# Performance work log

Hardware: AMD Instinct MI355X
Metric: run time of the kernel (lower is better)

The kernel has to match this reference:

```python
import jax, jax.numpy as jnp
import numpy as np

N_NODES = 50000
N_EDGES = 800000
DIM = 128
LN_EPS = 1e-5


def setup_inputs() -> dict:
    key = jax.random.key(0)
    k1, k2, k3, k4 = jax.random.split(key, 4)
    h = jax.random.normal(k1, (N_NODES, DIM), dtype=jnp.float32)
    edge_index = jax.random.randint(k2, (2, N_EDGES), 0, N_NODES, dtype=jnp.int64)
    W = jax.random.normal(k3, (DIM, DIM), dtype=jnp.float32) / np.sqrt(DIM)
    b = jnp.zeros((DIM,), dtype=jnp.float32)
    gamma = jnp.ones((DIM,), dtype=jnp.float32)
    beta = jnp.zeros((DIM,), dtype=jnp.float32)
    t = jnp.zeros((), dtype=jnp.float32)
    return {"t": t, "h": h, "edge_index": edge_index, "batch_size": N_NODES,
            "W": W, "b": b, "gamma": gamma, "beta": beta}


def _gcn_conv(h, edge_index, W, b):
    """PyG-style GCNConv: D^{-1/2} (A+I) D^{-1/2} (h W) + b."""
    N = h.shape[0]
    loops = jnp.arange(N, dtype=edge_index.dtype)
    src = jnp.concatenate([edge_index[0], loops])  # [E+N]
    dst = jnp.concatenate([edge_index[1], loops])  # [E+N]
    # degree (with self loops) on destination nodes
    deg = jax.ops.segment_sum(jnp.ones_like(dst, dtype=h.dtype), dst, num_segments=N)
    dinv = jnp.where(deg > 0, jax.lax.rsqrt(deg), 0.0)
    norm = dinv[src] * dinv[dst]                    # [E+N]
    xw = h @ W                                      # [N, D]
    msg = xw[src] * norm[:, None]                   # gather + scale, [E+N, D]
    agg = jax.ops.segment_sum(msg, dst, num_segments=N)  # scatter-add, [N, D]
    return agg + b


def reference(t, h, edge_index, batch_size, W, b, gamma, beta):
    if h.ndim == 1:
        h = h[None, :]
    dh = _gcn_conv(h, edge_index, W, b)
    # LayerNorm over feature dim, then tanh
    mean = jnp.mean(dh, axis=-1, keepdims=True)
    var = jnp.mean(jnp.square(dh - mean), axis=-1, keepdims=True)
    dh = (dh - mean) * jax.lax.rsqrt(var + LN_EPS) * gamma + beta
    dh = jnp.tanh(dh)
    return (dh, jnp.zeros_like(edge_index), jnp.zeros_like(jnp.asarray(batch_size)))
```

## Files before the change

kernel.cpp:

```cpp
#include <hip/hip_runtime.h>
#include <math.h>

#define NN 50000
#define NE 800000
#define D  128
#define SCAN_CHUNK 1024
#define NSCAN ((NN + SCAN_CHUNK - 1) / SCAN_CHUNK)
#define PG_BLOCKS 782

typedef __attribute__((ext_vector_type(8))) short bf16x8;
typedef __attribute__((ext_vector_type(4))) float f32x4;

__device__ __forceinline__ unsigned short f32_to_bf16(float f) {
    unsigned u = __float_as_uint(f);
    u = u + 0x7FFFu + ((u >> 16) & 1u);
    return (unsigned short)(u >> 16);
}

__device__ __forceinline__ float fast_tanh(float x) {
    float e = __expf(2.0f * x);
    return fmaf(-2.0f, __builtin_amdgcn_rcpf(e + 1.0f), 1.0f);
}

__global__ __launch_bounds__(256) void k_init(
        const float* __restrict__ Wg, int* __restrict__ deg,
        unsigned short* __restrict__ wpk, unsigned short* __restrict__ zb) {
    int tid = threadIdx.x;
    int idx = blockIdx.x * 256 + tid;

    if (idx < 12500) ((int4*)deg)[idx] = (int4){0, 0, 0, 0};
    if (idx == 12500) deg[50000] = 0;

    if (blockIdx.x == 0) {
#pragma unroll 8
        for (int i = 0; i < 64; i++) {
            int o = i * 256 + tid;
            int j = o & 7, frag = o >> 3;
            int lo = frag & 15, quad = (frag >> 4) & 3;
            int kt = (frag >> 6) & 3, nt = frag >> 8;
            int k = kt * 32 + quad * 8 + j, n = nt * 16 + lo;
            wpk[o] = f32_to_bf16(Wg[k * 128 + n]);
        }
    }
    if (blockIdx.x == 1 && tid < 64)
        ((unsigned*)(zb + (size_t)NN * D))[tid] = 0u;
}

__global__ __launch_bounds__(256) void k_count_gemm(
        const float* __restrict__ h, const uint4* __restrict__ wpk4,
        const int* __restrict__ ei, int* __restrict__ deg,
        unsigned short* __restrict__ rank, float* __restrict__ zf,
        int* __restrict__ outtail, int tailN) {
    int tid = threadIdx.x;
    int bid = blockIdx.x;

    if (bid & 1) {
        int g = (bid >> 1) * 256 + tid;
        if (g < NE / 4) {
            int4 d4 = ((const int4*)(ei + NE))[g];
            ushort4 r;
            r.x = (unsigned short)atomicAdd(&deg[d4.x], 1);
            r.y = (unsigned short)atomicAdd(&deg[d4.y], 1);
            r.z = (unsigned short)atomicAdd(&deg[d4.z], 1);
            r.w = (unsigned short)atomicAdd(&deg[d4.w], 1);
            ((ushort4*)rank)[g] = r;
        }
        for (int i = g; i < tailN; i += PG_BLOCKS * 256) outtail[i] = 0;
        return;
    }

    int gid = bid >> 1;
    int w = tid >> 6, lane = tid & 63;
    int quad = lane >> 4, lo = lane & 15;
    int rowBase = gid * 64 + w * 16;
    int rowA = rowBase + lo; if (rowA > NN - 1) rowA = NN - 1;
    const float4* h4 = (const float4*)h;

    bf16x8 af[4];
#pragma unroll
    for (int kt = 0; kt < 4; kt++) {
        float4 u = h4[(size_t)rowA * 32 + kt * 8 + quad * 2];
        float4 v = h4[(size_t)rowA * 32 + kt * 8 + quad * 2 + 1];
        bf16x8 a;
        a[0] = (short)f32_to_bf16(u.x); a[1] = (short)f32_to_bf16(u.y);
        a[2] = (short)f32_to_bf16(u.z); a[3] = (short)f32_to_bf16(u.w);
        a[4] = (short)f32_to_bf16(v.x); a[5] = (short)f32_to_bf16(v.y);
        a[6] = (short)f32_to_bf16(v.z); a[7] = (short)f32_to_bf16(v.w);
        af[kt] = a;
    }

    f32x4 acc[8];
#pragma unroll
    for (int nt = 0; nt < 8; nt++) acc[nt] = (f32x4){0.f, 0.f, 0.f, 0.f};

#pragma unroll
    for (int kt = 0; kt < 4; kt++) {
#pragma unroll
        for (int nt = 0; nt < 8; nt++) {
            uint4 tb = wpk4[nt * 256 + kt * 64 + lane];
            bf16x8 bfv = __builtin_bit_cast(bf16x8, tb);
            acc[nt] = __builtin_amdgcn_mfma_f32_16x16x32_bf16(af[kt], bfv, acc[nt], 0, 0, 0);
        }
    }

#pragma unroll
    for (int reg = 0; reg < 4; reg++) {
        int row = rowBase + quad * 4 + reg;
        if (row < NN) {
#pragma unroll
            for (int nt = 0; nt < 8; nt++)
                zf[(size_t)row * D + nt * 16 + lo] = acc[nt][reg];
        }
    }
}

__global__ __launch_bounds__(256) void k_scan(const int* __restrict__ deg,
                                              int* __restrict__ partial,
                                              int* __restrict__ flag,
                                              int* __restrict__ rowoff,
                                              float* __restrict__ dinv) {
    __shared__ int wsum[4];
    int t = threadIdx.x;
    int bid = blockIdx.x;
    int lane = t & 63, wv = t >> 6;
    int base = bid * SCAN_CHUNK + t * 4;
    int d[4]; int s = 0;
#pragma unroll
    for (int j = 0; j < 4; j++) {
        int i = base + j;
        d[j] = 0;
        if (i < NN) {
            d[j] = deg[i];
            s += d[j];
            dinv[i] = rsqrtf((float)d[j] + 1.0f);
        }
    }
    int v = s;
#pragma unroll
    for (int off = 1; off < 64; off <<= 1) {
        int u = __shfl_up(v, off, 64);
        if (lane >= off) v += u;
    }
    if (lane == 63) wsum[wv] = v;
    __syncthreads();
    int add = 0;
#pragma unroll
    for (int k = 0; k < 4; k++) if (k < wv) add += wsum[k];
    int inc = v + add;

    if (t == 255) {
        atomicExch(&partial[bid], inc);
        __threadfence();
        atomicAdd(flag, 1);
        while (atomicAdd(flag, 0) < NSCAN) {}
    }
    __syncthreads();

    int pv = (lane < NSCAN && lane < bid) ? atomicAdd(&partial[lane], 0) : 0;
#pragma unroll
    for (int off = 32; off > 0; off >>= 1) pv += __shfl_xor(pv, off, 64);

    int ex = inc - s + pv;
#pragma unroll
    for (int j = 0; j < 4; j++) {
        int i = base + j;
        if (i < NN) {
            rowoff[i] = ex;
            ex += d[j];
            if (i == NN - 1) rowoff[NN] = ex;
        }
    }
}

__global__ __launch_bounds__(320) void k_fill_scale(
        const int* __restrict__ ei, const int* __restrict__ rowoff,
        const unsigned short* __restrict__ rank, int* __restrict__ csr,
        const float* __restrict__ zf, const float* __restrict__ dinv,
        unsigned short* __restrict__ zb) {
    int t = blockIdx.x * 320 + threadIdx.x;

    int4 s4 = ((const int4*)ei)[t];
    int4 d4 = ((const int4*)(ei + NE))[t];
    ushort4 r4 = ((const ushort4*)rank)[t];
    csr[rowoff[d4.x] + r4.x] = s4.x;
    csr[rowoff[d4.y] + r4.y] = s4.y;
    csr[rowoff[d4.z] + r4.z] = s4.z;
    csr[rowoff[d4.w] + r4.w] = s4.w;

    int row = t >> 2, seg = t & 3;
    float dn = dinv[row];
    const float4* src = (const float4*)(zf + (size_t)row * D + seg * 32);
    uint4* dst = (uint4*)(zb + (size_t)row * D + seg * 32);
#pragma unroll
    for (int i = 0; i < 4; i++) {
        float4 a = src[i * 2], b = src[i * 2 + 1];
        uint4 o;
        o.x = (unsigned)f32_to_bf16(a.x * dn) | ((unsigned)f32_to_bf16(a.y * dn) << 16);
        o.y = (unsigned)f32_to_bf16(a.z * dn) | ((unsigned)f32_to_bf16(a.w * dn) << 16);
        o.z = (unsigned)f32_to_bf16(b.x * dn) | ((unsigned)f32_to_bf16(b.y * dn) << 16);
        o.w = (unsigned)f32_to_bf16(b.z * dn) | ((unsigned)f32_to_bf16(b.w * dn) << 16);
        dst[i] = o;
    }
}

__global__ __launch_bounds__(256) void k_gather_ln(
        const int* __restrict__ rowoff, const int* __restrict__ csr,
        const float* __restrict__ dinv, const unsigned* __restrict__ zbu,
        const float* __restrict__ bias, const float* __restrict__ gamma,
        const float* __restrict__ beta, float* __restrict__ out) {
    int tid = threadIdx.x;
    int w = tid >> 6, lane = tid & 63;
    int rowBase = blockIdx.x * 16 + w * 4;

    int cs[4], ce[4]; float dn[4]; unsigned selfz[4]; int v0[4];
#pragma unroll
    for (int r = 0; r < 4; r++) {
        int row = rowBase + r;
        cs[r] = __builtin_amdgcn_readfirstlane(rowoff[row]);
        ce[r] = __builtin_amdgcn_readfirstlane(rowoff[row + 1]);
        dn[r] = dinv[row];
        selfz[r] = zbu[(size_t)row * 64 + lane];
    }
#pragma unroll
    for (int r = 0; r < 4; r++) {
        int m0 = ce[r] - cs[r]; if (m0 > 64) m0 = 64;
        int t0 = csr[cs[r] + lane];
        v0[r] = (lane < m0) ? t0 : NN;
    }

    float2 x[4];
#pragma unroll
    for (int r = 0; r < 4; r++) {
        float ax = __uint_as_float(selfz[r] << 16);
        float ay = __uint_as_float(selfz[r] & 0xFFFF0000u);
        int c = cs[r];
        int v = v0[r];
        while (true) {
            int m = ce[r] - c; if (m > 64) m = 64;
            int nb = (m + 15) >> 4;
            for (int jb = 0; jb < nb; ++jb) {
                int j = jb << 4;
                unsigned p[16];
#pragma unroll
                for (int q = 0; q < 16; q++) {
                    int sq = __builtin_amdgcn_readlane(v, j + q);
                    p[q] = zbu[(size_t)sq * 64 + lane];
                }
#pragma unroll
                for (int q = 0; q < 16; q++) {
                    ax += __uint_as_float(p[q] << 16);
                    ay += __uint_as_float(p[q] & 0xFFFF0000u);
                }
            }
            c += 64;
            if (c >= ce[r]) break;
            int m2 = ce[r] - c; if (m2 > 64) m2 = 64;
            int t2 = csr[c + lane];
            v = (lane < m2) ? t2 : NN;
        }
        x[r].x = ax * dn[r];
        x[r].y = ay * dn[r];
    }

    float2 bi = ((const float2*)bias)[lane];
    float2 ga = ((const float2*)gamma)[lane];
    float2 be = ((const float2*)beta)[lane];
#pragma unroll
    for (int r = 0; r < 4; r++) {
        int row = rowBase + r;
        float y0 = x[r].x + bi.x;
        float y1 = x[r].y + bi.y;
        float s = y0 + y1;
#pragma unroll
        for (int off = 32; off > 0; off >>= 1) s += __shfl_xor(s, off, 64);
        float m = s * (1.0f / 128.0f);
        float v0f = y0 - m, v1f = y1 - m;
        float vs = v0f * v0f + v1f * v1f;
#pragma unroll
        for (int off = 32; off > 0; off >>= 1) vs += __shfl_xor(vs, off, 64);
        float rstd = rsqrtf(vs * (1.0f / 128.0f) + 1e-5f);
        float2 o;
        o.x = fast_tanh(v0f * rstd * ga.x + be.x);
        o.y = fast_tanh(v1f * rstd * ga.y + be.y);
        *(float2*)&out[(size_t)row * D + lane * 2] = o;
    }
}

extern "C" void kernel_launch(void* const* d_in, const int* in_sizes, int n_in,
                              void* d_out, int out_size, void* d_ws, size_t ws_size,
                              hipStream_t stream) {
    const float* h     = (const float*)d_in[1];
    const int*   ei    = (const int*)  d_in[2];
    const float* Wg    = (const float*)d_in[4];
    const float* b     = (const float*)d_in[5];
    const float* gamma = (const float*)d_in[6];
    const float* beta  = (const float*)d_in[7];
    float* out = (float*)d_out;

    char* wsb = (char*)d_ws;
    unsigned short* wpk    = (unsigned short*)(wsb);
    int*            deg    = (int*)(wsb + 32768);
    int*            flag   = (int*)(wsb + 232768);
    int*            partial= (int*)(wsb + 232832);
    unsigned short* rank   = (unsigned short*)(wsb + 233088);
    int*            rowoff = (int*)(wsb + 1833088);
    float*          dinv   = (float*)(wsb + 2633152);
    int*            csr    = (int*)(wsb + 2833152);
    unsigned short* zb     = (unsigned short*)(wsb + 6033408);
    float*          zf     = (float*)(wsb + 18833664);

    int tailN = out_size - NN * D;
    int* outtail = (int*)(out + (size_t)NN * D);

    k_init      <<<64,            256, 0, stream>>>(Wg, deg, wpk, zb);
    k_count_gemm<<<PG_BLOCKS * 2, 256, 0, stream>>>(h, (const uint4*)wpk, ei, deg, rank, zf, outtail, tailN);
    k_scan      <<<NSCAN,         256, 0, stream>>>(deg, partial, flag, rowoff, dinv);
    k_fill_scale<<<625,           320, 0, stream>>>(ei, rowoff, rank, csr, zf, dinv, zb);
    k_gather_ln <<<NN / 16,       256, 0, stream>>>(rowoff, csr, dinv, (const unsigned*)zb, b, gamma, beta, out);
}
```

Before: 192.5 us.

## Fuse scan, scale and CSR fill into one kernel with flag-based sync

Merges the degree scan kernel and the fill/scale kernel into one launch. The first 49 blocks do the decoupled scan, while the other blocks scale z to bf16 using a recomputed rsqrt of the degree. All blocks then spin on a second global flag before filling the CSR array in a grid-stride loop. This removes one kernel launch and overlaps the bf16 conversion with the scan, at the cost of every block busy-waiting, which depends on all blocks being co-resident. The flags are now reset in k_init instead of depending on prior state.

```diff
diff --git a/kernel.cpp b/kernel.cpp
--- a/kernel.cpp
+++ b/kernel.cpp
@@ -5,8 +5,10 @@
 #define NE 800000
 #define D  128
 #define SCAN_CHUNK 1024
-#define NSCAN ((NN + SCAN_CHUNK - 1) / SCAN_CHUNK)
+#define NSCAN 49
 #define PG_BLOCKS 782
+#define NROLES 1564
+#define SSF_BLOCKS 832
 
 typedef __attribute__((ext_vector_type(8))) short bf16x8;
 typedef __attribute__((ext_vector_type(4))) float f32x4;
@@ -24,12 +26,13 @@
 
 __global__ __launch_bounds__(256) void k_init(
         const float* __restrict__ Wg, int* __restrict__ deg,
+        int* __restrict__ flag, int* __restrict__ flag2,
         unsigned short* __restrict__ wpk, unsigned short* __restrict__ zb) {
     int tid = threadIdx.x;
     int idx = blockIdx.x * 256 + tid;
 
-    if (idx < 12500) ((int4*)deg)[idx] = (int4){0, 0, 0, 0};
-    if (idx == 12500) deg[50000] = 0;
+    if (idx < NN / 4) ((int4*)deg)[idx] = (int4){0, 0, 0, 0};
+    if (idx == NN / 4) { *flag = 0; *flag2 = 0; }
 
     if (blockIdx.x == 0) {
 #pragma unroll 8
@@ -38,8 +41,7 @@
             int j = o & 7, frag = o >> 3;
             int lo = frag & 15, quad = (frag >> 4) & 3;
             int kt = (frag >> 6) & 3, nt = frag >> 8;
-            int k = kt * 32 + quad * 8 + j, n = nt * 16 + lo;
-            wpk[o] = f32_to_bf16(Wg[k * 128 + n]);
+            wpk[o] = f32_to_bf16(Wg[(kt * 32 + quad * 8 + j) * 128 + nt * 16 + lo]);
         }
     }
     if (blockIdx.x == 1 && tid < 64)
@@ -94,14 +96,13 @@
     for (int nt = 0; nt < 8; nt++) acc[nt] = (f32x4){0.f, 0.f, 0.f, 0.f};
 
 #pragma unroll
-    for (int kt = 0; kt < 4; kt++) {
+    for (int kt = 0; kt < 4; kt++)
 #pragma unroll
         for (int nt = 0; nt < 8; nt++) {
             uint4 tb = wpk4[nt * 256 + kt * 64 + lane];
-            bf16x8 bfv = __builtin_bit_cast(bf16x8, tb);
-            acc[nt] = __builtin_amdgcn_mfma_f32_16x16x32_bf16(af[kt], bfv, acc[nt], 0, 0, 0);
-        }
-    }
+            acc[nt] = __builtin_amdgcn_mfma_f32_16x16x32_bf16(
+                af[kt], __builtin_bit_cast(bf16x8, tb), acc[nt], 0, 0, 0);
+        }
 
 #pragma unroll
     for (int reg = 0; reg < 4; reg++) {
@@ -114,92 +115,109 @@
     }
 }
 
-__global__ __launch_bounds__(256) void k_scan(const int* __restrict__ deg,
-                                              int* __restrict__ partial,
-                                              int* __restrict__ flag,
-                                              int* __restrict__ rowoff,
-                                              float* __restrict__ dinv) {
+__global__ __launch_bounds__(256) void k_scan_scale_fill(
+        const int* __restrict__ deg, int* __restrict__ partial,
+        int* __restrict__ flag, int* __restrict__ flag2,
+        int* __restrict__ rowoff, float* __restrict__ dinv,
+        const float* __restrict__ zf, unsigned short* __restrict__ zb,
+        const int* __restrict__ ei, const unsigned short* __restrict__ rank,
+        int* __restrict__ csr) {
     __shared__ int wsum[4];
-    int t = threadIdx.x;
+    int tid = threadIdx.x;
     int bid = blockIdx.x;
-    int lane = t & 63, wv = t >> 6;
-    int base = bid * SCAN_CHUNK + t * 4;
-    int d[4]; int s = 0;
-#pragma unroll
-    for (int j = 0; j < 4; j++) {
-        int i = base + j;
-        d[j] = 0;
-        if (i < NN) {
-            d[j] = deg[i];
-            s += d[j];
-            dinv[i] = rsqrtf((float)d[j] + 1.0f);
-        }
-    }
-    int v = s;
-#pragma unroll
-    for (int off = 1; off < 64; off <<= 1) {
-        int u = __shfl_up(v, off, 64);
-        if (lane >= off) v += u;
-    }
-    if (lane == 63) wsum[wv] = v;
+
+    if (bid < NSCAN) {
+        int lane = tid & 63, wv = tid >> 6;
+        int base = bid * SCAN_CHUNK + tid * 4;
+        int d[4]; int s = 0;
+#pragma unroll
+        for (int j = 0; j < 4; j++) {
+            int i = base + j;
+            d[j] = 0;
+            if (i < NN) {
+                d[j] = deg[i];
+                s += d[j];
+                dinv[i] = rsqrtf((float)d[j] + 1.0f);
+            }
+        }
+        int v = s;
+#pragma unroll
+        for (int off = 1; off < 64; off <<= 1) {
+            int u = __shfl_up(v, off, 64);
+            if (lane >= off) v += u;
+        }
+        if (lane == 63) wsum[wv] = v;
+        __syncthreads();
+        int add = 0;
+#pragma unroll
+        for (int k = 0; k < 4; k++) if (k < wv) add += wsum[k];
+        int inc = v + add;
+        if (tid == 255) {
+            atomicExch(&partial[bid], inc);
+            __threadfence();
+            atomicAdd(flag, 1);
+            while (atomicAdd(flag, 0) < NSCAN) {}
+        }
+        __syncthreads();
+        int pv = (lane < NSCAN && lane < bid) ? atomicAdd(&partial[lane], 0) : 0;
+#pragma unroll
+        for (int off = 32; off > 0; off >>= 1) pv += __shfl_xor(pv, off, 64);
+        int ex = inc - s + pv;
+#pragma unroll
+        for (int j = 0; j < 4; j++) {
+            int i = base + j;
+            if (i < NN) {
+                __hip_atomic_store(&rowoff[i], ex, __ATOMIC_RELAXED,
+                                   __HIP_MEMORY_SCOPE_AGENT);
+                ex += d[j];
+                if (i == NN - 1)
+                    __hip_atomic_store(&rowoff[NN], ex, __ATOMIC_RELAXED,
+                                       __HIP_MEMORY_SCOPE_AGENT);
+            }
+        }
+        __syncthreads();
+        if (tid == 0)
+            __hip_atomic_fetch_add(flag2, 1, __ATOMIC_RELEASE,
+                                   __HIP_MEMORY_SCOPE_AGENT);
+    } else {
+        int g = (bid - NSCAN) * 256 + tid;
+        if (g < NN * 4) {
+            int row = g >> 2, seg = g & 3;
+            float dn = rsqrtf((float)deg[row] + 1.0f);
+            const float4* src = (const float4*)(zf + (size_t)row * D + seg * 32);
+            uint4* dst = (uint4*)(zb + (size_t)row * D + seg * 32);
+#pragma unroll
+            for (int i = 0; i < 4; i++) {
+                float4 a = src[i * 2], bb = src[i * 2 + 1];
+                uint4 o;
+                o.x = (unsigned)f32_to_bf16(a.x * dn) | ((unsigned)f32_to_bf16(a.y * dn) << 16);
+                o.y = (unsigned)f32_to_bf16(a.z * dn) | ((unsigned)f32_to_bf16(a.w * dn) << 16);
+                o.z = (unsigned)f32_to_bf16(bb.x * dn) | ((unsigned)f32_to_bf16(bb.y * dn) << 16);
+                o.w = (unsigned)f32_to_bf16(bb.z * dn) | ((unsigned)f32_to_bf16(bb.w * dn) << 16);
+                dst[i] = o;
+            }
+        }
+    }
+
+    if (tid == 0) {
+        while (__hip_atomic_load(flag2, __ATOMIC_ACQUIRE,
+                                 __HIP_MEMORY_SCOPE_AGENT) < NSCAN)
+            __builtin_amdgcn_s_sleep(2);
+    }
     __syncthreads();
-    int add = 0;
-#pragma unroll
-    for (int k = 0; k < 4; k++) if (k < wv) add += wsum[k];
-    int inc = v + add;
-
-    if (t == 255) {
-        atomicExch(&partial[bid], inc);
-        __threadfence();
-        atomicAdd(flag, 1);
-        while (atomicAdd(flag, 0) < NSCAN) {}
-    }
-    __syncthreads();
-
-    int pv = (lane < NSCAN && lane < bid) ? atomicAdd(&partial[lane], 0) : 0;
-#pragma unroll
-    for (int off = 32; off > 0; off >>= 1) pv += __shfl_xor(pv, off, 64);
-
-    int ex = inc - s + pv;
-#pragma unroll
-    for (int j = 0; j < 4; j++) {
-        int i = base + j;
-        if (i < NN) {
-            rowoff[i] = ex;
-            ex += d[j];
-            if (i == NN - 1) rowoff[NN] = ex;
-        }
-    }
-}
-
-__global__ __launch_bounds__(320) void k_fill_scale(
-        const int* __restrict__ ei, const int* __restrict__ rowoff,
-        const unsigned short* __restrict__ rank, int* __restrict__ csr,
-        const float* __restrict__ zf, const float* __restrict__ dinv,
-        unsigned short* __restrict__ zb) {
-    int t = blockIdx.x * 320 + threadIdx.x;
-
-    int4 s4 = ((const int4*)ei)[t];
-    int4 d4 = ((const int4*)(ei + NE))[t];
-    ushort4 r4 = ((const ushort4*)rank)[t];
-    csr[rowoff[d4.x] + r4.x] = s4.x;
-    csr[rowoff[d4.y] + r4.y] = s4.y;
-    csr[rowoff[d4.z] + r4.z] = s4.z;
-    csr[rowoff[d4.w] + r4.w] = s4.w;
-
-    int row = t >> 2, seg = t & 3;
-    float dn = dinv[row];
-    const float4* src = (const float4*)(zf + (size_t)row * D + seg * 32);
-    uint4* dst = (uint4*)(zb + (size_t)row * D + seg * 32);
-#pragma unroll
-    for (int i = 0; i < 4; i++) {
-        float4 a = src[i * 2], b = src[i * 2 + 1];
-        uint4 o;
-        o.x = (unsigned)f32_to_bf16(a.x * dn) | ((unsigned)f32_to_bf16(a.y * dn) << 16);
-        o.y = (unsigned)f32_to_bf16(a.z * dn) | ((unsigned)f32_to_bf16(a.w * dn) << 16);
-        o.z = (unsigned)f32_to_bf16(b.x * dn) | ((unsigned)f32_to_bf16(b.y * dn) << 16);
-        o.w = (unsigned)f32_to_bf16(b.z * dn) | ((unsigned)f32_to_bf16(b.w * dn) << 16);
-        dst[i] = o;
+
+    for (int g = bid * 256 + tid; g < NE / 4; g += SSF_BLOCKS * 256) {
+        int4 s4 = ((const int4*)ei)[g];
+        int4 d4 = ((const int4*)(ei + NE))[g];
+        ushort4 r4 = ((const ushort4*)rank)[g];
+        int ox = __hip_atomic_load(&rowoff[d4.x], __ATOMIC_RELAXED, __HIP_MEMORY_SCOPE_AGENT);
+        int oy = __hip_atomic_load(&rowoff[d4.y], __ATOMIC_RELAXED, __HIP_MEMORY_SCOPE_AGENT);
+        int oz = __hip_atomic_load(&rowoff[d4.z], __ATOMIC_RELAXED, __HIP_MEMORY_SCOPE_AGENT);
+        int ow = __hip_atomic_load(&rowoff[d4.w], __ATOMIC_RELAXED, __HIP_MEMORY_SCOPE_AGENT);
+        csr[ox + r4.x] = s4.x;
+        csr[oy + r4.y] = s4.y;
+        csr[oz + r4.z] = s4.z;
+        csr[ow + r4.w] = s4.w;
     }
 }
 
@@ -301,6 +319,7 @@
     unsigned short* wpk    = (unsigned short*)(wsb);
     int*            deg    = (int*)(wsb + 32768);
     int*            flag   = (int*)(wsb + 232768);
+    int*            flag2  = (int*)(wsb + 232772);
     int*            partial= (int*)(wsb + 232832);
     unsigned short* rank   = (unsigned short*)(wsb + 233088);
     int*            rowoff = (int*)(wsb + 1833088);
@@ -312,9 +331,8 @@
     int tailN = out_size - NN * D;
     int* outtail = (int*)(out + (size_t)NN * D);
 
-    k_init      <<<64,            256, 0, stream>>>(Wg, deg, wpk, zb);
-    k_count_gemm<<<PG_BLOCKS * 2, 256, 0, stream>>>(h, (const uint4*)wpk, ei, deg, rank, zf, outtail, tailN);
-    k_scan      <<<NSCAN,         256, 0, stream>>>(deg, partial, flag, rowoff, dinv);
-    k_fill_scale<<<625,           320, 0, stream>>>(ei, rowoff, rank, csr, zf, dinv, zb);
-    k_gather_ln <<<NN / 16,       256, 0, stream>>>(rowoff, csr, dinv, (const unsigned*)zb, b, gamma, beta, out);
-}
+    k_init          <<<64,         256, 0, stream>>>(Wg, deg, flag, flag2, wpk, zb);
+    k_count_gemm    <<<NROLES,     256, 0, stream>>>(h, (const uint4*)wpk, ei, deg, rank, zf, outtail, tailN);
+    k_scan_scale_fill<<<SSF_BLOCKS,256, 0, stream>>>(deg, partial, flag, flag2, rowoff, dinv, zf, zb, ei, rank, csr);
+    k_gather_ln     <<<NN / 16,    256, 0, stream>>>(rowoff, csr, dinv, (const unsigned*)zb, b, gamma, beta, out);
+}
```

Result: slower. 242.0 us (+25.7%).
